# Kernel optimization log

Measured on AMD Instinct MI355X. Metric: run time of the kernel, lower is better.

The kernel has to match this reference:

```python
import jax, jax.numpy as jnp
import numpy as np

B, D, H = 64, 2048, 2048


def setup_inputs() -> dict:
    key = jax.random.key(0)
    ks = jax.random.split(key, 10)
    s = 1.0 / np.sqrt(D)  # Linear init scale
    # small z scale keeps exp() gates in a sane range
    return {
        "t": jnp.zeros((), jnp.float32),
        "z": jax.random.normal(ks[0], (B, D), jnp.float32) * 0.02,
        "K": jax.random.normal(ks[1], (B, D), jnp.float32) * 0.02,
        "V": jax.random.normal(ks[2], (B, D, D), jnp.float32) * 0.02,
        "Wq": jax.random.normal(ks[3], (D, D), jnp.float32) * s,
        "bq": jnp.zeros((D,), jnp.float32),
        "Wk": jax.random.normal(ks[4], (D, D), jnp.float32) * s,
        "bk": jnp.zeros((D,), jnp.float32),
        "Wv": jax.random.normal(ks[5], (D, D), jnp.float32) * s,
        "bv": jnp.zeros((D,), jnp.float32),
        "W1": jax.random.normal(ks[6], (D, H), jnp.float32) * s,
        "b1": jnp.zeros((H,), jnp.float32),
        "W2": jax.random.normal(ks[7], (H, D), jnp.float32) * (1.0 / np.sqrt(H)),
        "b2": jnp.zeros((D,), jnp.float32),
    }


def reference(t, z, K, V, Wq, bq, Wk, bk, Wv, bv, W1, b1, W2, b2):
    # get_ode_gradient_nn: 2-layer tanh MLP (stand-in for user ode_func_net)
    dz = jnp.tanh(z @ W1 + b1) @ W2 + b2                 # [B, D]
    dK = jnp.exp(z @ Wk + bk)                            # exp gate, [B, D]
    v = z @ Wv + bv                                      # [B, D]
    dV = jnp.einsum("bd,be->bde", v, dK)                # rank-1 outer update, [B, D, D]
    q = jnp.exp(z @ Wq + bq)                             # [B, D]
    a = jnp.sum(q * dK, axis=-1, keepdims=True)          # q . dK, [B, 1]
    dq = q * (dz @ Wq + bq)                              # [B, D]
    da = a + jnp.sum(dq * K, axis=-1, keepdims=True)     # [B, 1]
    dc = jnp.einsum("bde,be->bd", dV, q) + jnp.einsum("bde,be->bd", V, dq)  # [B, D]
    return (dz, da, dc, dK, dV)
```

## Files before the change

### kernel.cpp

```cpp
#include <hip/hip_runtime.h>
#include <cstddef>
#include <math.h>

#define BB 64
#define DD 2048
#define HH 2048
#define BD (BB*DD)
#define WN (2048*2048)

typedef unsigned short u16;
typedef __attribute__((ext_vector_type(8))) short bf16x8;
typedef __attribute__((ext_vector_type(4))) float f32x4;
typedef __attribute__((ext_vector_type(4))) float f4;

__device__ __forceinline__ u16 f2b(float x) {
    union { float f; unsigned u; } v; v.f = x;
    unsigned r = v.u + 0x7FFFu + ((v.u >> 16) & 1u);
    return (u16)(r >> 16);
}

__device__ __forceinline__ void gload16(const void* g, void* l) {
    __builtin_amdgcn_global_load_lds(
        (__attribute__((address_space(1))) void*)g,
        (__attribute__((address_space(3))) void*)l, 16, 0, 0);
}


__global__ __launch_bounds__(256) void wconv(
    const float* __restrict__ W0, const float* __restrict__ W1,
    const float* __restrict__ W2, const float* __restrict__ W3,
    const float* __restrict__ W4, u16* __restrict__ wt)
{
    const float* W;
    switch (blockIdx.z) {
        case 0: W = W0; break; case 1: W = W1; break;
        case 2: W = W2; break; case 3: W = W3; break;
        default: W = W4; break;
    }
    u16* T = wt + (size_t)blockIdx.z * WN;

    __shared__ u16 tile[64][66];
    int k0 = blockIdx.x * 64, n0 = blockIdx.y * 64;
    int t = threadIdx.x;
    {
        int r = t >> 2, c0 = (t & 3) * 16;
        const float* src = W + (size_t)(k0 + r) * DD + n0 + c0;
#pragma unroll
        for (int q = 0; q < 4; ++q) {
            float4 f = *(const float4*)(src + q * 4);
            tile[r][c0 + q*4 + 0] = f2b(f.x);
            tile[r][c0 + q*4 + 1] = f2b(f.y);
            tile[r][c0 + q*4 + 2] = f2b(f.z);
            tile[r][c0 + q*4 + 3] = f2b(f.w);
        }
    }
    __syncthreads();
    {
        int rn = t >> 2, ck = (t & 3) * 16;
        u16 o[16];
#pragma unroll
        for (int j = 0; j < 16; ++j) o[j] = tile[ck + j][rn];
        u16* dst = T + (size_t)(n0 + rn) * DD + k0 + ck;
        *(bf16x8*)dst       = *(bf16x8*)&o[0];
        *(bf16x8*)(dst + 8) = *(bf16x8*)&o[8];
    }
}

__global__ __launch_bounds__(256) void zconv(
    const float* __restrict__ z, u16* __restrict__ zb)
{
    int i = (blockIdx.x * 256 + threadIdx.x) * 4;
    float4 f = *(const float4*)&z[i];
    union { u16 u[4]; uint2 v; } o;
    o.u[0] = f2b(f.x); o.u[1] = f2b(f.y); o.u[2] = f2b(f.z); o.u[3] = f2b(f.w);
    *(uint2*)&zb[i] = o.v;
}

__device__ __forceinline__ void gemm_bf16_body(
    const u16* __restrict__ A, const u16* __restrict__ Wt,
    float* __restrict__ P, int kc)
{
    __shared__ u16 Als[64 * 32];
    __shared__ u16 Wls[64 * 32];
    const int t = threadIdx.x, w = t >> 6, lane = t & 63;
    const int n0 = blockIdx.x * 64;
    const int k0 = blockIdx.y * kc;

    f32x4 acc[4];
#pragma unroll
    for (int mt = 0; mt < 4; ++mt) acc[mt] = (f32x4){0.f, 0.f, 0.f, 0.f};

    const int srow = lane >> 2;
    const int sk   = (lane & 3) * 8;
    const u16* gA = A  + (size_t)(w * 16 + srow) * DD + k0 + sk;
    const u16* gW = Wt + (size_t)(n0 + w * 16 + srow) * DD + k0 + sk;
    u16* lA = &Als[w * 512];
    u16* lW = &Wls[w * 512];

    const int lane15 = lane & 15;
    const int k8 = (lane >> 4) * 8;

    for (int kk = 0; kk < kc; kk += 32) {
        gload16(gA, lA);
        gload16(gW, lW);
        gA += 32; gW += 32;
        __syncthreads();

        bf16x8 bfrag = *(const bf16x8*)&Wls[(w * 16 + lane15) * 32 + k8];
#pragma unroll
        for (int mt = 0; mt < 4; ++mt) {
            bf16x8 afrag = *(const bf16x8*)&Als[(mt * 16 + lane15) * 32 + k8];
            acc[mt] = __builtin_amdgcn_mfma_f32_16x16x32_bf16(
                afrag, bfrag, acc[mt], 0, 0, 0);
        }
        __syncthreads();
    }

    const int col = n0 + w * 16 + lane15;
    const int r4 = (lane >> 4) * 4;
#pragma unroll
    for (int mt = 0; mt < 4; ++mt)
#pragma unroll
        for (int j = 0; j < 4; ++j)
            P[(size_t)(mt * 16 + r4 + j) * DD + col] = acc[mt][j];
}

__global__ __launch_bounds__(256) void gemm_bf16_single(
    const u16* __restrict__ A, const u16* __restrict__ Wt,
    float* __restrict__ part, int kc)
{
    float* P = part + (size_t)blockIdx.y * 64 * DD;
    gemm_bf16_body(A, Wt, P, kc);
}

__global__ __launch_bounds__(256) void gemm_bf16_kv(
    const u16* __restrict__ A, const u16* __restrict__ Wkt,
    const u16* __restrict__ Wvt, float* __restrict__ p0,
    float* __restrict__ p1, int kc)
{
    const u16* Wt = blockIdx.z ? Wvt : Wkt;
    float* P = (blockIdx.z ? p1 : p0) + (size_t)blockIdx.y * 64 * DD;
    gemm_bf16_body(A, Wt, P, kc);
}

__global__ __launch_bounds__(256) void gemm_bf16_q(
    const u16* __restrict__ zb, const u16* __restrict__ dzb,
    const u16* __restrict__ Wqt, float* __restrict__ part, int kc)
{
    const u16* A = blockIdx.z ? dzb : zb;
    float* P = part + ((size_t)blockIdx.y * 128 + blockIdx.z * 64) * DD;
    gemm_bf16_body(A, Wqt, P, kc);
}

__global__ __launch_bounds__(256) void ep_h(
    const float* __restrict__ p, const float* __restrict__ b1,
    u16* __restrict__ hb, int KS)
{
    int i = blockIdx.x * 256 + threadIdx.x;
    float s = b1[i & (DD - 1)];
    for (int ks = 0; ks < KS; ++ks) s += p[(size_t)ks * BD + i];
    hb[i] = f2b(tanhf(s));
}

__global__ __launch_bounds__(256) void ep_dz(
    const float* __restrict__ p, const float* __restrict__ b2,
    float* __restrict__ dz, u16* __restrict__ dzb, int KS)
{
    int i = blockIdx.x * 256 + threadIdx.x;
    float s = b2[i & (DD - 1)];
    for (int ks = 0; ks < KS; ++ks) s += p[(size_t)ks * BD + i];
    dz[i]  = s;
    dzb[i] = f2b(s);
}

__global__ __launch_bounds__(256) void ep_kv(
    const float* __restrict__ pk, const float* __restrict__ pv,
    const float* __restrict__ bk, const float* __restrict__ bv,
    float* __restrict__ dKo, float* __restrict__ vo, int KS)
{
    int i = blockIdx.x * 256 + threadIdx.x;
    int d = i & (DD - 1);
    float sk = 0.f, sv = 0.f;
    for (int ks = 0; ks < KS; ++ks) {
        sk += pk[(size_t)ks * BD + i];
        sv += pv[(size_t)ks * BD + i];
    }
    dKo[i] = expf(sk + bk[d]);
    vo[i]  = sv + bv[d];
}

__global__ __launch_bounds__(256) void ep_q_dq(
    const float* __restrict__ pq, const float* __restrict__ bq,
    float* __restrict__ qo, float* __restrict__ dqo, int KS)
{
    int i = blockIdx.x * 256 + threadIdx.x;
    int b = i >> 11, d = i & (DD - 1);
    float sq = 0.f, sd = 0.f;
    for (int ks = 0; ks < KS; ++ks) {
        const float* P = pq + (size_t)ks * (128 * DD);
        sq += P[(size_t)b * DD + d];
        sd += P[(size_t)(b + 64) * DD + d];
    }
    float bb = bq[d];
    float qv = expf(sq + bb);
    qo[i]  = qv;
    dqo[i] = qv * (sd + bb);
}

template<int MT>
__device__ __forceinline__ void gemm_body_f32(
    const float* __restrict__ A0, const float* __restrict__ A1,
    const float* __restrict__ W, float* __restrict__ part, int kc)
{
    constexpr int KC = 32;
    constexpr int RT = MT / 16;
    __shared__ float As[KC][MT];
    __shared__ float Ws[KC][64];

    const int t  = threadIdx.x;
    const int n0 = blockIdx.x * 64;
    const int k0 = blockIdx.y * kc;
    const int i  = t >> 4;
    const int j  = t & 15;

    float acc[RT][4];
#pragma unroll
    for (int r = 0; r < RT; ++r)
#pragma unroll
        for (int c = 0; c < 4; ++c) acc[r][c] = 0.f;

    for (int kk0 = 0; kk0 < kc; kk0 += KC) {
        {
            int kk = t >> 3;
            int nn = (t & 7) << 3;
            const float* s = W + (size_t)(k0 + kk0 + kk) * DD + n0 + nn;
            *(float4*)&Ws[kk][nn]     = *(const float4*)s;
            *(float4*)&Ws[kk][nn + 4] = *(const float4*)(s + 4);
        }
        if constexpr (MT == 64) {
            int m  = t & 63;
            int kb = (t >> 6) << 3;
            const float* s = A0 + (size_t)m * DD + k0 + kk0 + kb;
            float4 a0 = *(const float4*)s;
            float4 a1 = *(const float4*)(s + 4);
            As[kb+0][m] = a0.x; As[kb+1][m] = a0.y;
            As[kb+2][m] = a0.z; As[kb+3][m] = a0.w;
            As[kb+4][m] = a1.x; As[kb+5][m] = a1.y;
            As[kb+6][m] = a1.z; As[kb+7][m] = a1.w;
        } else {
            int m  = t & 127;
            int kb = (t >> 7) << 4;
            const float* base = (m < 64) ? (A0 + (size_t)m * DD)
                                         : (A1 + (size_t)(m - 64) * DD);
            const float* s = base + k0 + kk0 + kb;
#pragma unroll
            for (int p = 0; p < 4; ++p) {
                float4 av = *(const float4*)(s + p * 4);
                As[kb+p*4+0][m] = av.x; As[kb+p*4+1][m] = av.y;
                As[kb+p*4+2][m] = av.z; As[kb+p*4+3][m] = av.w;
            }
        }
        __syncthreads();
#pragma unroll
        for (int kk = 0; kk < KC; ++kk) {
            float4 wv = *(float4*)&Ws[kk][j << 2];
#pragma unroll
            for (int rq = 0; rq < RT / 4; ++rq) {
                float4 av = *(float4*)&As[kk][i * RT + rq * 4];
                acc[rq*4+0][0] = fmaf(av.x, wv.x, acc[rq*4+0][0]);
                acc[rq*4+0][1] = fmaf(av.x, wv.y, acc[rq*4+0][1]);
                acc[rq*4+0][2] = fmaf(av.x, wv.z, acc[rq*4+0][2]);
                acc[rq*4+0][3] = fmaf(av.x, wv.w, acc[rq*4+0][3]);
                acc[rq*4+1][0] = fmaf(av.y, wv.x, acc[rq*4+1][0]);
                acc[rq*4+1][1] = fmaf(av.y, wv.y, acc[rq*4+1][1]);
                acc[rq*4+1][2] = fmaf(av.y, wv.z, acc[rq*4+1][2]);
                acc[rq*4+1][3] = fmaf(av.y, wv.w, acc[rq*4+1][3]);
                acc[rq*4+2][0] = fmaf(av.z, wv.x, acc[rq*4+2][0]);
                acc[rq*4+2][1] = fmaf(av.z, wv.y, acc[rq*4+2][1]);
                acc[rq*4+2][2] = fmaf(av.z, wv.z, acc[rq*4+2][2]);
                acc[rq*4+2][3] = fmaf(av.z, wv.w, acc[rq*4+2][3]);
                acc[rq*4+3][0] = fmaf(av.w, wv.x, acc[rq*4+3][0]);
                acc[rq*4+3][1] = fmaf(av.w, wv.y, acc[rq*4+3][1]);
                acc[rq*4+3][2] = fmaf(av.w, wv.z, acc[rq*4+3][2]);
                acc[rq*4+3][3] = fmaf(av.w, wv.w, acc[rq*4+3][3]);
            }
        }
        __syncthreads();
    }

    float* P = part + (size_t)blockIdx.y * MT * DD + n0 + (j << 2);
#pragma unroll
    for (int r = 0; r < RT; ++r)
        *(float4*)&P[(size_t)(i * RT + r) * DD] =
            make_float4(acc[r][0], acc[r][1], acc[r][2], acc[r][3]);
}

__global__ __launch_bounds__(256) void gemm64(
    const float* __restrict__ A, const float* __restrict__ W,
    float* __restrict__ part, int kc)
{ gemm_body_f32<64>(A, A, W, part, kc); }

__global__ __launch_bounds__(256) void gemm64_z2(
    const float* __restrict__ A,
    const float* __restrict__ W0, const float* __restrict__ W1,
    float* __restrict__ p0, float* __restrict__ p1, int kc)
{
    const float* W = blockIdx.z ? W1 : W0;
    float*       P = blockIdx.z ? p1 : p0;
    gemm_body_f32<64>(A, A, W, P, kc);
}

__global__ __launch_bounds__(256) void gemm128(
    const float* __restrict__ A0, const float* __restrict__ A1,
    const float* __restrict__ W, float* __restrict__ part, int kc)
{ gemm_body_f32<128>(A0, A1, W, part, kc); }

__global__ __launch_bounds__(256) void epilogue_f32(
    const float* __restrict__ part, const float* __restrict__ bias,
    float* __restrict__ out, int act, int KS)
{
    int i = blockIdx.x * 256 + threadIdx.x;
    float s = bias[i & (DD - 1)];
    for (int ks = 0; ks < KS; ++ks) s += part[(size_t)ks * BD + i];
    if (act == 1) s = tanhf(s);
    out[i] = s;
}

__global__ __launch_bounds__(256) void reduce_a_da(
    const float* __restrict__ q, const float* __restrict__ dK,
    const float* __restrict__ dq, const float* __restrict__ Kin,
    float* __restrict__ a_ws, float* __restrict__ da_out)
{
    int b = blockIdx.x;
    int t = threadIdx.x;
    const float* qb  = q   + (size_t)b * DD;
    const float* dKb = dK  + (size_t)b * DD;
    const float* dqb = dq  + (size_t)b * DD;
    const float* Kb  = Kin + (size_t)b * DD;

    float s1 = 0.f, s2 = 0.f;
    for (int i = t; i < DD; i += 256) {
        s1 = fmaf(qb[i],  dKb[i], s1);
        s2 = fmaf(dqb[i], Kb[i],  s2);
    }
#pragma unroll
    for (int off = 32; off; off >>= 1) {
        s1 += __shfl_down(s1, off);
        s2 += __shfl_down(s2, off);
    }
    __shared__ float r1[4], r2[4];
    if ((t & 63) == 0) { r1[t >> 6] = s1; r2[t >> 6] = s2; }
    __syncthreads();
    if (t == 0) {
        float a  = r1[0] + r1[1] + r1[2] + r1[3];
        float k2 = r2[0] + r2[1] + r2[2] + r2[3];
        a_ws[b]   = a;
        da_out[b] = a + k2;
    }
}

__global__ __launch_bounds__(256) void fused_dv_dc(
    const float* __restrict__ V, const float* __restrict__ v,
    const float* __restrict__ dK, const float* __restrict__ dq,
    const float* __restrict__ a, float* __restrict__ dV,
    float* __restrict__ dc)
{
    int b     = blockIdx.x >> 5;
    int chunk = blockIdx.x & 31;
    int wave  = threadIdx.x >> 6;
    int lane  = threadIdx.x & 63;

    const f4* dK4 = (const f4*)(dK + ((size_t)b << 11));
    const f4* dq4 = (const f4*)(dq + ((size_t)b << 11));
    f4 dKr[8], dqr[8];
#pragma unroll
    for (int u = 0; u < 8; ++u) {
        dKr[u] = dK4[u * 64 + lane];
        dqr[u] = dq4[u * 64 + lane];
    }
    float ab = a[b];
    int row0 = chunk * 64 + wave * 16;

    for (int g = 0; g < 4; ++g) {
        float dot[4];
#pragma unroll
        for (int r2 = 0; r2 < 4; ++r2) {
            int row = row0 + g * 4 + r2;
            size_t off = ((size_t)((b << 11) | row)) << 11;
            const f4* V4  = (const f4*)(V  + off);
            f4*       dV4 = (f4*)(dV + off);
            float vr = v[((size_t)b << 11) + row];
            float d  = 0.f;
#pragma unroll
            for (int u = 0; u < 8; ++u) {
                f4 Vv = __builtin_nontemporal_load(&V4[u * 64 + lane]);
                d += Vv[0] * dqr[u][0] + Vv[1] * dqr[u][1]
                   + Vv[2] * dqr[u][2] + Vv[3] * dqr[u][3];
                f4 o = vr * dKr[u];
                __builtin_nontemporal_store(o, &dV4[u * 64 + lane]);
            }
            dot[r2] = d;
        }
#pragma unroll
        for (int r2 = 0; r2 < 4; ++r2) {
            float d = dot[r2];
#pragma unroll
            for (int s = 32; s; s >>= 1) d += __shfl_down(d, s);
            if (lane == 0) {
                int row = row0 + g * 4 + r2;
                dc[((size_t)b << 11) + row] =
                    v[((size_t)b << 11) + row] * ab + d;
            }
        }
    }
}

extern "C" void kernel_launch(void* const* d_in, const int* in_sizes, int n_in,
                              void* d_out, int out_size, void* d_ws, size_t ws_size,
                              hipStream_t stream)
{
    const float* z   = (const float*)d_in[1];
    const float* Kin = (const float*)d_in[2];
    const float* Vin = (const float*)d_in[3];
    const float* Wq  = (const float*)d_in[4];
    const float* bq  = (const float*)d_in[5];
    const float* Wk  = (const float*)d_in[6];
    const float* bk  = (const float*)d_in[7];
    const float* Wv  = (const float*)d_in[8];
    const float* bv  = (const float*)d_in[9];
    const float* W1  = (const float*)d_in[10];
    const float* b1  = (const float*)d_in[11];
    const float* W2  = (const float*)d_in[12];
    const float* b2  = (const float*)d_in[13];

    float* out   = (float*)d_out;
    float* o_dz  = out;
    float* o_da  = out + BD;
    float* o_dc  = out + BD + BB;
    float* o_dK  = out + 2 * BD + BB;
    float* o_dV  = out + 3 * BD + BB;

    float* ws    = (float*)d_ws;
    float* ws_v  = ws;
    float* ws_q  = ws + BD;
    float* ws_dq = ws + 2 * BD;
    float* ws_a  = ws + 3 * BD;
    float* ws_h  = ws + 3 * BD + 64;
    u16*   zb    = (u16*)(ws + 4 * BD + 64);
    u16*   hb    = zb + BD;
    u16*   dzb   = hb + BD;
    u16*   wt    = dzb + BD;
    float* poolb = (float*)(wt + 5ull * WN);

    const size_t pre_fl = 4ull * BD + 64 + (3ull * BD + 5ull * WN) / 2;

    int KS = 0;
    for (int ks = 16; ks >= 4; ks >>= 1)
        if ((pre_fl + 2ull * ks * BD) * 4ull <= ws_size) { KS = ks; break; }

    dim3 blk(256);
    dim3 gE(BD / 256);

    if (KS) {
        int kc = DD / KS;
        float* p0 = poolb;
        float* p1 = poolb + (size_t)KS * BD;

        dim3 gW(32, 32, 5);
        dim3 gG(32, KS);
        dim3 gG2(32, KS, 2);

        wconv<<<gW, blk, 0, stream>>>(W1, W2, Wk, Wv, Wq, wt);
        zconv<<<dim3(BD / 1024), blk, 0, stream>>>(z, zb);

        u16* W1t = wt;
        u16* W2t = wt + 1ull * WN;
        u16* Wkt = wt + 2ull * WN;
        u16* Wvt = wt + 3ull * WN;
        u16* Wqt = wt + 4ull * WN;

        gemm_bf16_single<<<gG, blk, 0, stream>>>(zb, W1t, p0, kc);
        ep_h<<<gE, blk, 0, stream>>>(p0, b1, hb, KS);

        gemm_bf16_single<<<gG, blk, 0, stream>>>(hb, W2t, p0, kc);
        ep_dz<<<gE, blk, 0, stream>>>(p0, b2, o_dz, dzb, KS);

        gemm_bf16_kv<<<gG2, blk, 0, stream>>>(zb, Wkt, Wvt, p0, p1, kc);
        ep_kv<<<gE, blk, 0, stream>>>(p0, p1, bk, bv, o_dK, ws_v, KS);

        gemm_bf16_q<<<gG2, blk, 0, stream>>>(zb, dzb, Wqt, p0, kc);
        ep_q_dq<<<gE, blk, 0, stream>>>(p0, bq, ws_q, ws_dq, KS);
    } else {
        float* pool = ws + 4 * BD + 64;
        int KSf = 16;
        while (KSf > 1 &&
               ((size_t)(4 * BD + 64) + 2ull * KSf * BD) * 4ull > ws_size)
            KSf >>= 1;
        int kc = DD / KSf;
        float* p0 = pool;
        float* p1 = pool + (size_t)KSf * BD;

        dim3 gG(DD / 64, KSf);
        dim3 gG2(DD / 64, KSf, 2);

        gemm64<<<gG, blk, 0, stream>>>(z, W1, p0, kc);
        epilogue_f32<<<gE, blk, 0, stream>>>(p0, b1, ws_h, 1, KSf);

        gemm64<<<gG, blk, 0, stream>>>(ws_h, W2, p0, kc);
        epilogue_f32<<<gE, blk, 0, stream>>>(p0, b2, o_dz, 0, KSf);

        gemm64_z2<<<gG2, blk, 0, stream>>>(z, Wk, Wv, p0, p1, kc);
        ep_kv<<<gE, blk, 0, stream>>>(p0, p1, bk, bv, o_dK, ws_v, KSf);

        gemm128<<<gG, blk, 0, stream>>>(z, o_dz, Wq, p0, kc);
        ep_q_dq<<<gE, blk, 0, stream>>>(p0, bq, ws_q, ws_dq, KSf);
    }

    reduce_a_da<<<dim3(BB), blk, 0, stream>>>(ws_q, o_dK, ws_dq, Kin, ws_a, o_da);

    fused_dv_dc<<<dim3(BB * 32), blk, 0, stream>>>(Vin, ws_v, o_dK, ws_dq, ws_a,
                                                   o_dV, o_dc);
}
```

Baseline: 493.9 us.

## Double-buffer GEMM LDS with swizzle, fold zconv into wconv, simplify dV loop

The split-K bf16 GEMM body now uses two LDS buffers, prefetching the next K tile while MFMAs run on the current one, and applies an XOR swizzle to LDS columns to reduce bank conflicts. The z-to-bf16 conversion is merged into the weight-conversion kernel as an extra grid slice, removing one launch. The dV/dc streaming kernel drops its nontemporal loads and stores and grouped reductions in favour of a plain per-row loop. The shown loop no longer has a trailing __syncthreads, which risks a race on buffer reuse unless one exists in hidden code. Plain caching of the large V/dV streams may also affect cache behaviour.

```diff
diff --git a/kernel.cpp b/kernel.cpp
--- a/kernel.cpp
+++ b/kernel.cpp
@@ -29,8 +29,24 @@
 __global__ __launch_bounds__(256) void wconv(
     const float* __restrict__ W0, const float* __restrict__ W1,
     const float* __restrict__ W2, const float* __restrict__ W3,
-    const float* __restrict__ W4, u16* __restrict__ wt)
-{
+    const float* __restrict__ W4, u16* __restrict__ wt,
+    const float* __restrict__ z, u16* __restrict__ zb)
+{
+    int t = threadIdx.x;
+    if (blockIdx.z == 5) {
+        if (blockIdx.y != 0 || blockIdx.x >= 32) return;
+        int i0 = blockIdx.x * 4096 + t * 16;
+        u16 o[16];
+#pragma unroll
+        for (int q = 0; q < 4; ++q) {
+            float4 f = *(const float4*)&z[i0 + q * 4];
+            o[q*4+0] = f2b(f.x); o[q*4+1] = f2b(f.y);
+            o[q*4+2] = f2b(f.z); o[q*4+3] = f2b(f.w);
+        }
+        *(bf16x8*)&zb[i0]     = *(bf16x8*)&o[0];
+        *(bf16x8*)&zb[i0 + 8] = *(bf16x8*)&o[8];
+        return;
+    }
     const float* W;
     switch (blockIdx.z) {
         case 0: W = W0; break; case 1: W = W1; break;
@@ -41,7 +57,6 @@
 
     __shared__ u16 tile[64][66];
     int k0 = blockIdx.x * 64, n0 = blockIdx.y * 64;
-    int t = threadIdx.x;
     {
         int r = t >> 2, c0 = (t & 3) * 16;
         const float* src = W + (size_t)(k0 + r) * DD + n0 + c0;
@@ -66,22 +81,12 @@
     }
 }
 
-__global__ __launch_bounds__(256) void zconv(
-    const float* __restrict__ z, u16* __restrict__ zb)
-{
-    int i = (blockIdx.x * 256 + threadIdx.x) * 4;
-    float4 f = *(const float4*)&z[i];
-    union { u16 u[4]; uint2 v; } o;
-    o.u[0] = f2b(f.x); o.u[1] = f2b(f.y); o.u[2] = f2b(f.z); o.u[3] = f2b(f.w);
-    *(uint2*)&zb[i] = o.v;
-}
-
 __device__ __forceinline__ void gemm_bf16_body(
     const u16* __restrict__ A, const u16* __restrict__ Wt,
     float* __restrict__ P, int kc)
 {
-    __shared__ u16 Als[64 * 32];
-    __shared__ u16 Wls[64 * 32];
+    __shared__ u16 Als[2][64 * 32];
+    __shared__ u16 Wls[2][64 * 32];
     const int t = threadIdx.x, w = t >> 6, lane = t & 63;
     const int n0 = blockIdx.x * 64;
     const int k0 = blockIdx.y * kc;
@@ -91,25 +96,29 @@
     for (int mt = 0; mt < 4; ++mt) acc[mt] = (f32x4){0.f, 0.f, 0.f, 0.f};
 
     const int srow = lane >> 2;
-    const int sk   = (lane & 3) * 8;
-    const u16* gA = A  + (size_t)(w * 16 + srow) * DD + k0 + sk;
-    const u16* gW = Wt + (size_t)(n0 + w * 16 + srow) * DD + k0 + sk;
-    u16* lA = &Als[w * 512];
-    u16* lW = &Wls[w * 512];
+    const int csrc = (lane & 3) ^ ((lane >> 3) & 3);
+    const u16* gA = A  + (size_t)(w * 16 + srow) * DD + k0 + csrc * 8;
+    const u16* gW = Wt + (size_t)(n0 + w * 16 + srow) * DD + k0 + csrc * 8;
 
     const int lane15 = lane & 15;
-    const int k8 = (lane >> 4) * 8;
-
-    for (int kk = 0; kk < kc; kk += 32) {
-        gload16(gA, lA);
-        gload16(gW, lW);
-        gA += 32; gW += 32;
-        __syncthreads();
-
-        bf16x8 bfrag = *(const bf16x8*)&Wls[(w * 16 + lane15) * 32 + k8];
+    const int cread  = lane >> 4;
+    const int swz    = (cread ^ ((lane15 >> 1) & 3)) << 3;
+
+    const int nt = kc >> 5;
+    gload16(gA, &Als[0][w * 512]);
+    gload16(gW, &Wls[0][w * 512]);
+    __syncthreads();
+
+    for (int it = 0; it < nt; ++it) {
+        const int cur = it & 1;
+        if (it + 1 < nt) {
+            gload16(gA + (size_t)(it + 1) * 32, &Als[cur ^ 1][w * 512]);
+            gload16(gW + (size_t)(it + 1) * 32, &Wls[cur ^ 1][w * 512]);
+        }
+        bf16x8 bfrag = *(const bf16x8*)&Wls[cur][(w * 16 + lane15) * 32 + swz];
 #pragma unroll
         for (int mt = 0; mt < 4; ++mt) {
-            bf16x8 afrag = *(const bf16x8*)&Als[(mt * 16 + lane15) * 32 + k8];
+            bf16x8 afrag = *(const bf16x8*)&Als[cur][(mt * 16 + lane15) * 32 + swz];
             acc[mt] = __builtin_amdgcn_mfma_f32_16x16x32_bf16(
                 afrag, bfrag, acc[mt], 0, 0, 0);
         }
@@ -379,39 +388,27 @@
         dqr[u] = dq4[u * 64 + lane];
     }
     float ab = a[b];
+
     int row0 = chunk * 64 + wave * 16;
-
-    for (int g = 0; g < 4; ++g) {
-        float dot[4];
-#pragma unroll
-        for (int r2 = 0; r2 < 4; ++r2) {
-            int row = row0 + g * 4 + r2;
-            size_t off = ((size_t)((b << 11) | row)) << 11;
-            const f4* V4  = (const f4*)(V  + off);
-            f4*       dV4 = (f4*)(dV + off);
-            float vr = v[((size_t)b << 11) + row];
-            float d  = 0.f;
-#pragma unroll
-            for (int u = 0; u < 8; ++u) {
-                f4 Vv = __builtin_nontemporal_load(&V4[u * 64 + lane]);
-                d += Vv[0] * dqr[u][0] + Vv[1] * dqr[u][1]
-                   + Vv[2] * dqr[u][2] + Vv[3] * dqr[u][3];
-                f4 o = vr * dKr[u];
-                __builtin_nontemporal_store(o, &dV4[u * 64 + lane]);
-            }
-            dot[r2] = d;
-        }
-#pragma unroll
-        for (int r2 = 0; r2 < 4; ++r2) {
-            float d = dot[r2];
-#pragma unroll
-            for (int s = 32; s; s >>= 1) d += __shfl_down(d, s);
-            if (lane == 0) {
-                int row = row0 + g * 4 + r2;
-                dc[((size_t)b << 11) + row] =
-                    v[((size_t)b << 11) + row] * ab + d;
-            }
-        }
+    for (int rr = 0; rr < 16; ++rr) {
+        int row = row0 + rr;
+        size_t off = ((size_t)((b << 11) | row)) << 11;
+        const f4* V4  = (const f4*)(V  + off);
+        f4*       dV4 = (f4*)(dV + off);
+
+        float dot = 0.f;
+        float vr = v[((size_t)b << 11) + row];
+#pragma unroll
+        for (int u = 0; u < 8; ++u) {
+            f4 Vv = V4[u * 64 + lane];
+            dot += Vv[0] * dqr[u][0] + Vv[1] * dqr[u][1]
+                 + Vv[2] * dqr[u][2] + Vv[3] * dqr[u][3];
+            f4 o = vr * dKr[u];
+            dV4[u * 64 + lane] = o;
+        }
+#pragma unroll
+        for (int s = 32; s; s >>= 1) dot += __shfl_down(dot, s);
+        if (lane == 0) dc[((size_t)b << 11) + row] = vr * ab + dot;
     }
 }
 
@@ -466,12 +463,11 @@
         float* p0 = poolb;
         float* p1 = poolb + (size_t)KS * BD;
 
-        dim3 gW(32, 32, 5);
+        dim3 gW(32, 32, 6);
         dim3 gG(32, KS);
         dim3 gG2(32, KS, 2);
 
-        wconv<<<gW, blk, 0, stream>>>(W1, W2, Wk, Wv, Wq, wt);
-        zconv<<<dim3(BD / 1024), blk, 0, stream>>>(z, zb);
+        wconv<<<gW, blk, 0, stream>>>(W1, W2, Wk, Wv, Wq, wt, z, zb);
 
         u16* W1t = wt;
         u16* W2t = wt + 1ull * WN;
```

Result: slower. 533.6 us (+8.0%).
